# Performance work log

Hardware: AMD Instinct MI355X
Metric: run time of the kernel (lower is better)

The kernel has to match this reference:

```python
import jax, jax.numpy as jnp
import numpy as np

M, D, I, E, TOPK = 2048, 1024, 2048, 8, 2

def setup_inputs() -> dict:
    key = jax.random.key(0)
    k1, k2, k3, k4 = jax.random.split(key, 4)
    x = jax.random.normal(k1, (M, D), dtype=jnp.float32)
    w13 = jax.random.normal(k2, (E, 2 * I, D), dtype=jnp.float32) * 0.02
    w2 = jax.random.normal(k3, (E, D, I), dtype=jnp.float32) * 0.02
    expert_indices = jax.random.randint(k4, (M, TOPK), 0, E, dtype=jnp.int64)
    return {"x": x, "w13": w13, "w2": w2, "expert_indices": expert_indices}

def reference(x, w13, w2, expert_indices):
    # Faithful to the 'gpt-fast' math: per (token, slot) SiLU-gated expert FFN.
    # Instead of gathering per-token weight copies (huge), compute each expert's
    # FFN densely over all tokens, then gather the selected expert output.
    inter = w2.shape[2]

    def per_expert(w13_e, w2_e):
        h = jnp.einsum('md,nd->mn', x, w13_e)          # [M, 2I]
        x1, x3 = h[:, :inter], h[:, inter:]
        return jnp.einsum('mi,di->md', jax.nn.silu(x1) * x3, w2_e)  # [M, D]

    outs = jax.vmap(per_expert)(w13, w2)               # [E, M, D]
    outs = jnp.transpose(outs, (1, 0, 2))              # [M, E, D]
    # out[t, a] = outs[t, expert_indices[t, a]]
    idx = expert_indices[..., None]                    # [M, TOPK, 1]
    return jnp.take_along_axis(outs, idx, axis=1)      # [M, TOPK, D]
```

## Files before the change

kernel.cpp:

```cpp
#include <hip/hip_runtime.h>
#include <hip/hip_bf16.h>
#include <cstdint>
#include <cstddef>

#define DDIM  1024
#define IDIM  2048
#define NEXP  8
#define NPAIR 4096
#define MAXTILE 40

typedef __attribute__((ext_vector_type(8))) short short8;
typedef __attribute__((ext_vector_type(4))) float floatx4;
typedef __attribute__((ext_vector_type(4))) float fvec4;

__device__ inline short8 pack8v(fvec4 a, fvec4 b) {
    union { short8 s8; __hip_bfloat162 h[4]; } u;
    u.h[0] = __float22bfloat162_rn(float2{a.x, a.y});
    u.h[1] = __float22bfloat162_rn(float2{a.z, a.w});
    u.h[2] = __float22bfloat162_rn(float2{b.x, b.y});
    u.h[3] = __float22bfloat162_rn(float2{b.z, b.w});
    return u.s8;
}

__device__ inline void gload_lds16(const unsigned short* g, unsigned short* l) {
    __builtin_amdgcn_global_load_lds((const __attribute__((address_space(1))) void*)g,
                                     (__attribute__((address_space(3))) void*)l, 16, 0, 0);
}

__launch_bounds__(256)
__global__ void cvt_all(const fvec4* __restrict__ x, const fvec4* __restrict__ w13,
                        const fvec4* __restrict__ w2,
                        uint4* __restrict__ xb, uint4* __restrict__ w13b,
                        uint4* __restrict__ w2b) {
    const int t = threadIdx.x;
    for (int job = blockIdx.x; job < 6400; job += gridDim.x) {
        const fvec4* src; uint4* dst; int cbase;
        if (job < 4096)      { src = w13; dst = w13b; cbase = job << 10; }
        else if (job < 6144) { src = w2;  dst = w2b;  cbase = (job - 4096) << 10; }
        else                 { src = x;   dst = xb;   cbase = (job - 6144) << 10; }
        const int c0 = cbase + t;
        fvec4 a0 = __builtin_nontemporal_load(src + 2 * (c0 + 0));
        fvec4 b0 = __builtin_nontemporal_load(src + 2 * (c0 + 0) + 1);
        fvec4 a1 = __builtin_nontemporal_load(src + 2 * (c0 + 256));
        fvec4 b1 = __builtin_nontemporal_load(src + 2 * (c0 + 256) + 1);
        fvec4 a2 = __builtin_nontemporal_load(src + 2 * (c0 + 512));
        fvec4 b2 = __builtin_nontemporal_load(src + 2 * (c0 + 512) + 1);
        fvec4 a3 = __builtin_nontemporal_load(src + 2 * (c0 + 768));
        fvec4 b3 = __builtin_nontemporal_load(src + 2 * (c0 + 768) + 1);
        __builtin_amdgcn_sched_barrier(0);
        short8 p0 = pack8v(a0, b0);
        short8 p1 = pack8v(a1, b1);
        short8 p2 = pack8v(a2, b2);
        short8 p3 = pack8v(a3, b3);
        dst[c0 + 0]   = *(uint4*)&p0;
        dst[c0 + 256] = *(uint4*)&p1;
        dst[c0 + 512] = *(uint4*)&p2;
        dst[c0 + 768] = *(uint4*)&p3;
    }
}

__global__ void route_kernel(const int* __restrict__ eidx,
                             int4* __restrict__ tbl,
                             int* __restrict__ slot_q) {
    __shared__ int cnt[NEXP];
    __shared__ int cur[NEXP];
    const int t = threadIdx.x;
    if (t < NEXP) cnt[t] = 0;
    __syncthreads();
    for (int q = t; q < NPAIR; q += 1024) atomicAdd(&cnt[eidx[q]], 1);
    __syncthreads();
    if (t == 0) {
        int s = 0, nt = 0;
        for (int e = 0; e < NEXP; e++) {
            cur[e] = s;
            for (int mb = 0; mb < cnt[e]; mb += 128)
                tbl[nt++] = int4{e, mb, s, cnt[e]};
            s += cnt[e];
        }
        for (; nt < MAXTILE; nt++) tbl[nt] = int4{0, 0, 0, 0};
    }
    __syncthreads();
    for (int q = t; q < NPAIR; q += 1024) {
        int e = eidx[q];
        int pos = atomicAdd(&cur[e], 1);
        slot_q[pos] = q;
    }
}

__launch_bounds__(256)
__global__ void gemm1_swiglu(const unsigned short* __restrict__ xb,
                             const unsigned short* __restrict__ w13b,
                             const int4* __restrict__ tbl,
                             const int* __restrict__ slot_q,
                             unsigned short* __restrict__ pbuf) {
    const int4 tt = tbl[blockIdx.y];
    const int e = tt.x, mbase = tt.y, off0 = tt.z, ne = tt.w;
    if (mbase >= ne) return;
    const int n0 = blockIdx.x * 64;

    __shared__ __align__(16) unsigned short As[2][128 * 64];
    __shared__ __align__(16) unsigned short Bs[2][128 * 64];

    const int t    = threadIdx.x;
    const int lane = t & 63;
    const int wid  = t >> 6;

    const int rr = t >> 3;
    const int g  = (t & 7) ^ (rr & 7);
    const unsigned short* pA[4];
    const unsigned short* pB[4];
    const unsigned short* wb1 = w13b + (size_t)e * (2 * IDIM) * DDIM;
    #pragma unroll
    for (int c = 0; c < 4; c++) {
        int row = c * 32 + rr;
        int sl = mbase + row; if (sl > ne - 1) sl = ne - 1;
        pA[c] = xb + (size_t)(slot_q[off0 + sl] >> 1) * DDIM + g * 8;
        int wrow = (row < 64) ? (n0 + row) : (IDIM + n0 + (row - 64));
        pB[c] = wb1 + (size_t)wrow * DDIM + g * 8;
    }
    const int lo = wid * 512;

    const int wm = wid >> 1, wn = wid & 1;
    const int quad = lane >> 4, l16 = lane & 15;
    const int rsw = l16 & 7;
    const int co0 = (quad ^ rsw) * 8;
    const int co1 = ((quad + 4) ^ rsw) * 8;

    floatx4 acc1[4][2], acc3[4][2];
    #pragma unroll
    for (int i = 0; i < 4; i++)
        #pragma unroll
        for (int j = 0; j < 2; j++) {
            acc1[i][j] = floatx4{0.f, 0.f, 0.f, 0.f};
            acc3[i][j] = floatx4{0.f, 0.f, 0.f, 0.f};
        }

    #pragma unroll
    for (int c = 0; c < 4; c++) {
        gload_lds16(pA[c], &As[0][lo + c * 2048]);
        gload_lds16(pB[c], &Bs[0][lo + c * 2048]);
    }
    asm volatile("s_waitcnt vmcnt(0)" ::: "memory");
    __builtin_amdgcn_s_barrier();
    __builtin_amdgcn_sched_barrier(0);

    int cur = 0;
    for (int it = 0; it < DDIM / 64; ++it) {
        if (it + 1 < DDIM / 64) {
            const int ko = (it + 1) * 64;
            #pragma unroll
            for (int c = 0; c < 4; c++) {
                gload_lds16(pA[c] + ko, &As[cur ^ 1][lo + c * 2048]);
                gload_lds16(pB[c] + ko, &Bs[cur ^ 1][lo + c * 2048]);
            }
        }
        __builtin_amdgcn_s_setprio(1);
        #pragma unroll
        for (int h = 0; h < 2; ++h) {
            const int co = h ? co1 : co0;
            short8 af[4], b1f[2], b3f[2];
            #pragma unroll
            for (int mi = 0; mi < 4; mi++)
                af[mi] = *(short8*)&As[cur][(wm * 64 + mi * 16 + l16) * 64 + co];
            #pragma unroll
            for (int ni = 0; ni < 2; ni++) {
                b1f[ni] = *(short8*)&Bs[cur][(wn * 32 + ni * 16 + l16) * 64 + co];
                b3f[ni] = *(short8*)&Bs[cur][(64 + wn * 32 + ni * 16 + l16) * 64 + co];
            }
            #pragma unroll
            for (int mi = 0; mi < 4; mi++)
                #pragma unroll
                for (int ni = 0; ni < 2; ni++) {
                    acc1[mi][ni] = __builtin_amdgcn_mfma_f32_16x16x32_bf16(af[mi], b1f[ni], acc1[mi][ni], 0, 0, 0);
                    acc3[mi][ni] = __builtin_amdgcn_mfma_f32_16x16x32_bf16(af[mi], b3f[ni], acc3[mi][ni], 0, 0, 0);
                }
        }
        __builtin_amdgcn_s_setprio(0);
        asm volatile("s_waitcnt vmcnt(0)" ::: "memory");
        __builtin_amdgcn_s_barrier();
        __builtin_amdgcn_sched_barrier(0);
        cur ^= 1;
    }

    #pragma unroll
    for (int mi = 0; mi < 4; mi++) {
        #pragma unroll
        for (int ni = 0; ni < 2; ni++) {
            const int col = n0 + wn * 32 + ni * 16 + l16;
            #pragma unroll
            for (int rw = 0; rw < 4; rw++) {
                const int s2 = mbase + wm * 64 + mi * 16 + quad * 4 + rw;
                if (s2 < ne) {
                    float v1 = acc1[mi][ni][rw];
                    float v3 = acc3[mi][ni][rw];
                    float pv = v1 / (1.f + __expf(-v1)) * v3;
                    __hip_bfloat16 pb = __float2bfloat16(pv);
                    pbuf[(size_t)(off0 + s2) * IDIM + col] = *(unsigned short*)&pb;
                }
            }
        }
    }
}

__launch_bounds__(256)
__global__ void gemm2_out(const unsigned short* __restrict__ pbuf,
                          const unsigned short* __restrict__ w2b,
                          const int4* __restrict__ tbl,
                          const int* __restrict__ slot_q,
                          float* __restrict__ out) {
    const int4 tt = tbl[blockIdx.y];
    const int e = tt.x, mbase = tt.y, off0 = tt.z, ne = tt.w;
    if (mbase >= ne) return;
    const int n0 = blockIdx.x * 64;

    __shared__ __align__(16) unsigned short As[2][128 * 64];
    __shared__ __align__(16) unsigned short Bs[2][64 * 64];

    const int t    = threadIdx.x;
    const int lane = t & 63;
    const int wid  = t >> 6;

    const int rr = t >> 3;
    const int g  = (t & 7) ^ (rr & 7);
    const unsigned short* pA[4];
    const unsigned short* pB[2];
    const unsigned short* wb = w2b + (size_t)e * DDIM * IDIM;
    #pragma unroll
    for (int c = 0; c < 4; c++) {
        int row = c * 32 + rr;
        int sl = mbase + row; if (sl > ne - 1) sl = ne - 1;
        pA[c] = pbuf + (size_t)(off0 + sl) * IDIM + g * 8;
    }
    #pragma unroll
    for (int c = 0; c < 2; c++) {
        int row = c * 32 + rr;
        pB[c] = wb + (size_t)(n0 + row) * IDIM + g * 8;
    }
    const int lo = wid * 512;

    const int wm = wid >> 1, wn = wid & 1;
    const int quad = lane >> 4, l16 = lane & 15;
    const int rsw = l16 & 7;
    const int co0 = (quad ^ rsw) * 8;
    const int co1 = ((quad + 4) ^ rsw) * 8;

    floatx4 acc[4][2];
    #pragma unroll
    for (int i = 0; i < 4; i++)
        #pragma unroll
        for (int j = 0; j < 2; j++) acc[i][j] = floatx4{0.f, 0.f, 0.f, 0.f};

    #pragma unroll
    for (int c = 0; c < 4; c++)
        gload_lds16(pA[c], &As[0][lo + c * 2048]);
    #pragma unroll
    for (int c = 0; c < 2; c++)
        gload_lds16(pB[c], &Bs[0][lo + c * 2048]);
    asm volatile("s_waitcnt vmcnt(0)" ::: "memory");
    __builtin_amdgcn_s_barrier();
    __builtin_amdgcn_sched_barrier(0);

    int cur = 0;
    for (int it = 0; it < IDIM / 64; ++it) {
        if (it + 1 < IDIM / 64) {
            const int ko = (it + 1) * 64;
            #pragma unroll
            for (int c = 0; c < 4; c++)
                gload_lds16(pA[c] + ko, &As[cur ^ 1][lo + c * 2048]);
            #pragma unroll
            for (int c = 0; c < 2; c++)
                gload_lds16(pB[c] + ko, &Bs[cur ^ 1][lo + c * 2048]);
        }
        __builtin_amdgcn_s_setprio(1);
        #pragma unroll
        for (int h = 0; h < 2; ++h) {
            const int co = h ? co1 : co0;
            short8 af[4], bf[2];
            #pragma unroll
            for (int mi = 0; mi < 4; mi++)
                af[mi] = *(short8*)&As[cur][(wm * 64 + mi * 16 + l16) * 64 + co];
            #pragma unroll
            for (int ni = 0; ni < 2; ni++)
                bf[ni] = *(short8*)&Bs[cur][(wn * 32 + ni * 16 + l16) * 64 + co];
            #pragma unroll
            for (int mi = 0; mi < 4; mi++)
                #pragma unroll
                for (int ni = 0; ni < 2; ni++)
                    acc[mi][ni] = __builtin_amdgcn_mfma_f32_16x16x32_bf16(af[mi], bf[ni], acc[mi][ni], 0, 0, 0);
        }
        __builtin_amdgcn_s_setprio(0);
        asm volatile("s_waitcnt vmcnt(0)" ::: "memory");
        __builtin_amdgcn_s_barrier();
        __builtin_amdgcn_sched_barrier(0);
        cur ^= 1;
    }

    #pragma unroll
    for (int mi = 0; mi < 4; mi++) {
        #pragma unroll
        for (int rw = 0; rw < 4; rw++) {
            const int s2 = mbase + wm * 64 + mi * 16 + quad * 4 + rw;
            if (s2 < ne) {
                const int qq = slot_q[off0 + s2];
                float* orow = out + (size_t)qq * DDIM;
                #pragma unroll
                for (int ni = 0; ni < 2; ni++)
                    orow[n0 + wn * 32 + ni * 16 + l16] = acc[mi][ni][rw];
            }
        }
    }
}

extern "C" void kernel_launch(void* const* d_in, const int* in_sizes, int n_in,
                              void* d_out, int out_size, void* d_ws, size_t ws_size,
                              hipStream_t stream) {
    const float* x    = (const float*)d_in[0];
    const float* w13  = (const float*)d_in[1];
    const float* w2   = (const float*)d_in[2];
    const int*   eidx = (const int*)d_in[3];
    float* out = (float*)d_out;

    const size_t OFF_XB   = 65536;
    const size_t OFF_W13B = OFF_XB + (size_t)4 * 1024 * 1024;
    const size_t OFF_W2B  = OFF_W13B + (size_t)64 * 1024 * 1024;
    const size_t OFF_PBUF = OFF_W2B + (size_t)32 * 1024 * 1024;

    int4* tbl   = (int4*)((char*)d_ws + 128);
    int* slot_q = (int*)((char*)d_ws + 1024);
    unsigned short* xb   = (unsigned short*)((char*)d_ws + OFF_XB);
    unsigned short* w13b = (unsigned short*)((char*)d_ws + OFF_W13B);
    unsigned short* w2b  = (unsigned short*)((char*)d_ws + OFF_W2B);
    unsigned short* pbuf = (unsigned short*)((char*)d_ws + OFF_PBUF);

    hipLaunchKernelGGL(route_kernel, dim3(1), dim3(1024), 0, stream, eidx, tbl, slot_q);
    hipLaunchKernelGGL(cvt_all, dim3(6400), dim3(256), 0, stream,
                       (const fvec4*)x, (const fvec4*)w13, (const fvec4*)w2,
                       (uint4*)xb, (uint4*)w13b, (uint4*)w2b);
    hipLaunchKernelGGL(gemm1_swiglu, dim3(IDIM / 64, MAXTILE), dim3(256), 0, stream,
                       xb, w13b, tbl, slot_q, pbuf);
    hipLaunchKernelGGL(gemm2_out, dim3(DDIM / 64, MAXTILE), dim3(256), 0, stream,
                       pbuf, w2b, tbl, slot_q, out);
}
```

Measured before the change: 344.0 us.

## Widen gemm1 tile to 128 columns with 512 threads, retune gemm2 wait

gemm1_swiglu now uses 512-thread blocks that each cover 128 intermediate columns (256 rows of w13), so every x tile loaded into LDS feeds twice as many outputs. To fit LDS it drops the double-buffered prefetch and uses a single buffer with two __syncthreads per k-step, which exposes load latency. gemm2_out swaps the trailing full vmcnt(0) wait for a partial vmcnt(6) wait after issuing the next prefetch, plus a barrier before compute, so the prefetch can overlap the current tile's MFMA work.

```diff
diff --git a/kernel.cpp b/kernel.cpp
--- a/kernel.cpp
+++ b/kernel.cpp
@@ -87,7 +87,7 @@
     }
 }
 
-__launch_bounds__(256)
+__launch_bounds__(512)
 __global__ void gemm1_swiglu(const unsigned short* __restrict__ xb,
                              const unsigned short* __restrict__ w13b,
                              const int4* __restrict__ tbl,
@@ -96,10 +96,10 @@
     const int4 tt = tbl[blockIdx.y];
     const int e = tt.x, mbase = tt.y, off0 = tt.z, ne = tt.w;
     if (mbase >= ne) return;
-    const int n0 = blockIdx.x * 64;
-
-    __shared__ __align__(16) unsigned short As[2][128 * 64];
-    __shared__ __align__(16) unsigned short Bs[2][128 * 64];
+    const int n0 = blockIdx.x * 128;
+
+    __shared__ __align__(16) unsigned short As[128 * 64];
+    __shared__ __align__(16) unsigned short Bs[256 * 64];
 
     const int t    = threadIdx.x;
     const int lane = t & 63;
@@ -107,20 +107,25 @@
 
     const int rr = t >> 3;
     const int g  = (t & 7) ^ (rr & 7);
-    const unsigned short* pA[4];
+    const unsigned short* pA[2];
     const unsigned short* pB[4];
     const unsigned short* wb1 = w13b + (size_t)e * (2 * IDIM) * DDIM;
     #pragma unroll
-    for (int c = 0; c < 4; c++) {
-        int row = c * 32 + rr;
+    for (int c = 0; c < 2; c++) {
+        int row = c * 64 + rr;
         int sl = mbase + row; if (sl > ne - 1) sl = ne - 1;
         pA[c] = xb + (size_t)(slot_q[off0 + sl] >> 1) * DDIM + g * 8;
-        int wrow = (row < 64) ? (n0 + row) : (IDIM + n0 + (row - 64));
+    }
+    #pragma unroll
+    for (int c = 0; c < 4; c++) {
+        int row = c * 64 + rr;
+        int wrow = (row < 128) ? (n0 + row) : (IDIM + n0 + (row - 128));
         pB[c] = wb1 + (size_t)wrow * DDIM + g * 8;
     }
-    const int lo = wid * 512;
-
-    const int wm = wid >> 1, wn = wid & 1;
+    unsigned short* lA = As + wid * 512;
+    unsigned short* lB = Bs + wid * 512;
+
+    const int wm = wid >> 2, wn = wid & 3;
     const int quad = lane >> 4, l16 = lane & 15;
     const int rsw = l16 & 7;
     const int co0 = (quad ^ rsw) * 8;
@@ -135,37 +140,28 @@
             acc3[i][j] = floatx4{0.f, 0.f, 0.f, 0.f};
         }
 
-    #pragma unroll
-    for (int c = 0; c < 4; c++) {
-        gload_lds16(pA[c], &As[0][lo + c * 2048]);
-        gload_lds16(pB[c], &Bs[0][lo + c * 2048]);
-    }
-    asm volatile("s_waitcnt vmcnt(0)" ::: "memory");
-    __builtin_amdgcn_s_barrier();
-    __builtin_amdgcn_sched_barrier(0);
-
-    int cur = 0;
     for (int it = 0; it < DDIM / 64; ++it) {
-        if (it + 1 < DDIM / 64) {
-            const int ko = (it + 1) * 64;
-            #pragma unroll
-            for (int c = 0; c < 4; c++) {
-                gload_lds16(pA[c] + ko, &As[cur ^ 1][lo + c * 2048]);
-                gload_lds16(pB[c] + ko, &Bs[cur ^ 1][lo + c * 2048]);
-            }
-        }
-        __builtin_amdgcn_s_setprio(1);
+        const int ko = it * 64;
+        __syncthreads();
+        #pragma unroll
+        for (int c = 0; c < 2; c++)
+            gload_lds16(pA[c] + ko, lA + c * 4096);
+        #pragma unroll
+        for (int c = 0; c < 4; c++)
+            gload_lds16(pB[c] + ko, lB + c * 4096);
+        __syncthreads();
+
         #pragma unroll
         for (int h = 0; h < 2; ++h) {
             const int co = h ? co1 : co0;
             short8 af[4], b1f[2], b3f[2];
             #pragma unroll
             for (int mi = 0; mi < 4; mi++)
-                af[mi] = *(short8*)&As[cur][(wm * 64 + mi * 16 + l16) * 64 + co];
+                af[mi] = *(short8*)&As[(wm * 64 + mi * 16 + l16) * 64 + co];
             #pragma unroll
             for (int ni = 0; ni < 2; ni++) {
-                b1f[ni] = *(short8*)&Bs[cur][(wn * 32 + ni * 16 + l16) * 64 + co];
-                b3f[ni] = *(short8*)&Bs[cur][(64 + wn * 32 + ni * 16 + l16) * 64 + co];
+                b1f[ni] = *(short8*)&Bs[(wn * 32 + ni * 16 + l16) * 64 + co];
+                b3f[ni] = *(short8*)&Bs[(128 + wn * 32 + ni * 16 + l16) * 64 + co];
             }
             #pragma unroll
             for (int mi = 0; mi < 4; mi++)
@@ -175,11 +171,6 @@
                     acc3[mi][ni] = __builtin_amdgcn_mfma_f32_16x16x32_bf16(af[mi], b3f[ni], acc3[mi][ni], 0, 0, 0);
                 }
         }
-        __builtin_amdgcn_s_setprio(0);
-        asm volatile("s_waitcnt vmcnt(0)" ::: "memory");
-        __builtin_amdgcn_s_barrier();
-        __builtin_amdgcn_sched_barrier(0);
-        cur ^= 1;
     }
 
     #pragma unroll
@@ -256,8 +247,6 @@
     #pragma unroll
     for (int c = 0; c < 2; c++)
         gload_lds16(pB[c], &Bs[0][lo + c * 2048]);
-    asm volatile("s_waitcnt vmcnt(0)" ::: "memory");
-    __builtin_amdgcn_s_barrier();
     __builtin_amdgcn_sched_barrier(0);
 
     int cur = 0;
@@ -270,7 +259,14 @@
             #pragma unroll
             for (int c = 0; c < 2; c++)
                 gload_lds16(pB[c] + ko, &Bs[cur ^ 1][lo + c * 2048]);
-        }
+            __builtin_amdgcn_sched_barrier(0);
+            asm volatile("s_waitcnt vmcnt(6)" ::: "memory");
+        } else {
+            asm volatile("s_waitcnt vmcnt(0)" ::: "memory");
+        }
+        __builtin_amdgcn_s_barrier();
+        __builtin_amdgcn_sched_barrier(0);
+
         __builtin_amdgcn_s_setprio(1);
         #pragma unroll
         for (int h = 0; h < 2; ++h) {
@@ -289,7 +285,6 @@
                     acc[mi][ni] = __builtin_amdgcn_mfma_f32_16x16x32_bf16(af[mi], bf[ni], acc[mi][ni], 0, 0, 0);
         }
         __builtin_amdgcn_s_setprio(0);
-        asm volatile("s_waitcnt vmcnt(0)" ::: "memory");
         __builtin_amdgcn_s_barrier();
         __builtin_amdgcn_sched_barrier(0);
         cur ^= 1;
@@ -336,7 +331,7 @@
     hipLaunchKernelGGL(cvt_all, dim3(6400), dim3(256), 0, stream,
                        (const fvec4*)x, (const fvec4*)w13, (const fvec4*)w2,
                        (uint4*)xb, (uint4*)w13b, (uint4*)w2b);
-    hipLaunchKernelGGL(gemm1_swiglu, dim3(IDIM / 64, MAXTILE), dim3(256), 0, stream,
+    hipLaunchKernelGGL(gemm1_swiglu, dim3(IDIM / 128, MAXTILE), dim3(512), 0, stream,
                        xb, w13b, tbl, slot_q, pbuf);
     hipLaunchKernelGGL(gemm2_out, dim3(DDIM / 64, MAXTILE), dim3(256), 0, stream,
                        pbuf, w2b, tbl, slot_q, out);
```

After: 335.7 us. 2.4% less time.
